# Kernel optimization log

Measured on AMD Instinct MI355X. Metric: run time of the kernel, lower is better.

## Reference

```python
import jax, jax.numpy as jnp
import numpy as np

NUM_ITEMS = 50000
NUM_USERS = 16384   # static number of user segments (total_user universe)
H0 = 512            # encoder_hidden_size[0]
LAT = 256           # bottleneck (encoder_hidden_size[-1] / decoder_hidden_size[0])
N = 262144          # observed interactions
NT = 262144         # target interactions


def setup_inputs() -> dict:
    key = jax.random.key(0)
    ks = jax.random.split(key, 14)

    def glorot(k, shape):
        fan_in, fan_out = shape[1], shape[0]
        lim = np.sqrt(6.0 / (fan_in + fan_out)).astype(np.float32)
        return jax.random.uniform(k, shape, jnp.float32, -lim, lim)

    return {
        "user": jax.random.randint(ks[0], (N,), 0, NUM_USERS, jnp.int32),
        "item": jax.random.randint(ks[1], (N,), 0, NUM_ITEMS, jnp.int32),
        "rating": jax.random.normal(ks[2], (N,), jnp.float32),
        "target_user": jax.random.randint(ks[3], (NT,), 0, NUM_USERS, jnp.int32),
        "target_item": jax.random.randint(ks[4], (NT,), 0, NUM_ITEMS, jnp.int32),
        "target_rating": jax.random.normal(ks[5], (NT,), jnp.float32),
        # encoder_linear: Linear(num_items, H0)
        "W_enc": glorot(ks[6], (H0, NUM_ITEMS)),
        "b_enc": jnp.zeros((H0,), jnp.float32),
        # Encoder: Linear(H0, LAT) + Tanh
        "W1": glorot(ks[7], (LAT, H0)),
        "b1": jnp.zeros((LAT,), jnp.float32),
        # Decoder: Linear(LAT, H0) + Tanh
        "W2": glorot(ks[8], (H0, LAT)),
        "b2": jnp.zeros((H0,), jnp.float32),
        # decoder_linear: Linear(H0, num_items)
        "W_dec": glorot(ks[9], (NUM_ITEMS, H0)),
        "b_dec": jnp.zeros((NUM_ITEMS,), jnp.float32),
    }


def reference(user, item, rating, target_user, target_item, target_rating,
              W_enc, b_enc, W1, b1, W2, b2, W_dec, b_dec):
    # --- encoder: gather item weight rows, scale by rating, segment-sum per user ---
    # rows: [N, H0] gather from W_enc.T ([NUM_ITEMS, H0])
    rows = W_enc.T[item] * rating[:, None]
    # per-user aggregation over the full user universe (equivalent to the
    # torch unique/sort/index_add path: users with no interactions get 0 -> tanh(bias))
    agg = jax.ops.segment_sum(rows, user, num_segments=NUM_USERS)  # [U, H0]
    x = jnp.tanh(agg + b_enc)
    # --- small dense tanh MLP encoder/decoder ---
    encoded = jnp.tanh(x @ W1.T + b1)          # [U, LAT]
    decoded = jnp.tanh(encoded @ W2.T + b2)    # [U, H0] (dropout = identity, eval mode)
    # --- decoder: gather user codes & item decoder rows, rowwise dot ---
    g = decoded[target_user]                   # [NT, H0]
    w = W_dec[target_item]                     # [NT, H0]
    pred = jnp.sum(g * w, axis=-1) + b_dec[target_item]  # [NT]
    loss = jnp.mean((pred - target_rating) ** 2)
    return pred, loss
```

## Files before the change

### kernel.cpp

```cpp
#include <hip/hip_runtime.h>
#include <hip/hip_bf16.h>
#include <math.h>

#define NUM_ITEMS 50000
#define NUM_USERS 16384
#define ITEM_BINS 65536
#define H0 512
#define LAT 256

typedef __attribute__((ext_vector_type(8))) short short8;
typedef __attribute__((ext_vector_type(4))) float floatx4;

__device__ __forceinline__ unsigned short f2bf(float f) {
    union { float f; unsigned i; } u; u.f = f;
    unsigned r = u.i + 0x7fff + ((u.i >> 16) & 1);
    return (unsigned short)(r >> 16);
}
__device__ __forceinline__ float bfhi(unsigned v) {
    union { unsigned i; float f; } u; u.i = v & 0xffff0000u; return u.f;
}
__device__ __forceinline__ float bflo(unsigned v) {
    union { unsigned i; float f; } u; u.i = v << 16; return u.f;
}
__device__ __forceinline__ uint4 pack8(const float* v) {
    uint4 p;
    p.x = (unsigned)f2bf(v[0]) | ((unsigned)f2bf(v[1]) << 16);
    p.y = (unsigned)f2bf(v[2]) | ((unsigned)f2bf(v[3]) << 16);
    p.z = (unsigned)f2bf(v[4]) | ((unsigned)f2bf(v[5]) << 16);
    p.w = (unsigned)f2bf(v[6]) | ((unsigned)f2bf(v[7]) << 16);
    return p;
}

__global__ __launch_bounds__(256) void setup_kernel(
        const float* __restrict__ W_enc, unsigned short* __restrict__ wtb,
        const float* __restrict__ W_dec, unsigned short* __restrict__ wdb,
        const float* __restrict__ W1, unsigned short* __restrict__ w1b,
        const float* __restrict__ W2, unsigned short* __restrict__ w2b,
        const int* __restrict__ user, int* __restrict__ cntU,
        const int* __restrict__ t_item, int* __restrict__ cntI,
        int n, int nt, int TB, int DB, int CB) {
    __shared__ float tile[64][65];
    int bid = blockIdx.x;
    int tid = threadIdx.x;
    if (bid < TB) {
        const int TBX = (NUM_ITEMS + 63) / 64;
        int bx = bid % TBX, by = bid / TBX;
        int x0 = bx * 64, y0 = by * 64;
        int tx = tid & 63, ty = tid >> 6;
        int x = x0 + tx;
        if (x < NUM_ITEMS) {
#pragma unroll
            for (int j = 0; j < 64; j += 4)
                tile[j + ty][tx] = W_enc[(size_t)(y0 + j + ty) * NUM_ITEMS + x];
        }
        __syncthreads();
#pragma unroll
        for (int j = 0; j < 64; j += 4) {
            int it = x0 + j + ty;
            if (it < NUM_ITEMS)
                wtb[(size_t)it * H0 + y0 + tx] = f2bf(tile[tx][j + ty]);
        }
    } else if (bid < TB + DB) {
        int idx = (bid - TB) * 2048 + tid * 8;
        float v[8];
        *(float4*)&v[0] = *(const float4*)(W_dec + idx);
        *(float4*)&v[4] = *(const float4*)(W_dec + idx + 4);
        *(uint4*)(wdb + idx) = pack8(v);
    } else if (bid < TB + DB + CB) {
        int i = (bid - TB - DB) * 1024 + tid * 4;
        if (i + 3 < n) {
            int4 u = *(const int4*)(user + i);
            atomicAdd(&cntU[u.x], 1); atomicAdd(&cntU[u.y], 1);
            atomicAdd(&cntU[u.z], 1); atomicAdd(&cntU[u.w], 1);
        } else {
            for (int k = i; k < n; ++k) atomicAdd(&cntU[user[k]], 1);
        }
        if (i + 3 < nt) {
            int4 t = *(const int4*)(t_item + i);
            atomicAdd(&cntI[t.x], 1); atomicAdd(&cntI[t.y], 1);
            atomicAdd(&cntI[t.z], 1); atomicAdd(&cntI[t.w], 1);
        } else {
            for (int k = i; k < nt; ++k) atomicAdd(&cntI[t_item[k]], 1);
        }
    } else {
        int b2i = bid - TB - DB - CB;
        const float* src = (b2i < 64) ? W1 : W2;
        unsigned short* dst = (b2i < 64) ? w1b : w2b;
        int idx = (b2i & 63) * 2048 + tid * 8;
        float v[8];
        *(float4*)&v[0] = *(const float4*)(src + idx);
        *(float4*)&v[4] = *(const float4*)(src + idx + 4);
        *(uint4*)(dst + idx) = pack8(v);
    }
}

__device__ void scan_block(const int* __restrict__ cnt, int* __restrict__ offs,
                           int* __restrict__ cursor, int per) {
    __shared__ int ssum[1024];
    int t = threadIdx.x;
    int base = t * per;
    int s = 0;
    for (int j = 0; j < per; j += 4) {
        int4 v = *(const int4*)(cnt + base + j);
        s += v.x + v.y + v.z + v.w;
    }
    ssum[t] = s;
    __syncthreads();
    for (int off = 1; off < 1024; off <<= 1) {
        int v = (t >= off) ? ssum[t - off] : 0;
        __syncthreads();
        ssum[t] += v;
        __syncthreads();
    }
    int run = (t == 0) ? 0 : ssum[t - 1];
    for (int j = 0; j < per; j += 4) {
        int4 v = *(const int4*)(cnt + base + j);
        int4 o;
        o.x = run; run += v.x;
        o.y = run; run += v.y;
        o.z = run; run += v.z;
        o.w = run; run += v.w;
        *(int4*)(offs + base + j) = o;
        *(int4*)(cursor + base + j) = o;
    }
}

__global__ void scan_kernel(const int* __restrict__ cntU, int* __restrict__ offsU, int* __restrict__ curU,
                            const int* __restrict__ cntI, int* __restrict__ offsI, int* __restrict__ curI) {
    if (blockIdx.x == 0) scan_block(cntU, offsU, curU, NUM_USERS / 1024);
    else scan_block(cntI, offsI, curI, ITEM_BINS / 1024);
}

__global__ void scatter_kernel(const int* __restrict__ user, const int* __restrict__ item,
                               const float* __restrict__ rating, int* __restrict__ curU,
                               int2* __restrict__ s_pack,
                               const int* __restrict__ t_user, const int* __restrict__ t_item,
                               const float* __restrict__ t_rating, int* __restrict__ curI,
                               int4* __restrict__ st_pack, int n, int nt) {
    int i = blockIdx.x * blockDim.x + threadIdx.x;
    if (i < n) {
        int u = user[i];
        int pos = atomicAdd(&curU[u], 1);
        s_pack[pos] = make_int2(item[i], __float_as_int(rating[i]));
    }
    if (i < nt) {
        int it = t_item[i];
        int pos = atomicAdd(&curI[it], 1);
        st_pack[pos] = make_int4(t_user[i], it, __float_as_int(t_rating[i]), i);
    }
}

__global__ __launch_bounds__(256) void agg_kernel(const unsigned short* __restrict__ wtb,
                                                  const int* __restrict__ offs,
                                                  const int* __restrict__ ends,
                                                  const int2* __restrict__ s_pack,
                                                  const float* __restrict__ b_enc,
                                                  unsigned short* __restrict__ xb) {
    __shared__ float red[3 * 512];
    int u = blockIdx.x;
    int tid = threadIdx.x;
    int g = tid >> 6, lane = tid & 63;
    float acc[8] = {};
    int j0 = offs[u], j1 = ends[u];
    int j = j0 + g;
    int2 nxt = (j < j1) ? s_pack[j] : make_int2(0, 0);
    while (j < j1) {
        int2 cur = nxt;
        int jn = j + 4;
        if (jn < j1) nxt = s_pack[jn];
        float r = __int_as_float(cur.y);
        uint4 v = ((const uint4*)(wtb + (size_t)cur.x * H0))[lane];
        acc[0] += bflo(v.x) * r; acc[1] += bfhi(v.x) * r;
        acc[2] += bflo(v.y) * r; acc[3] += bfhi(v.y) * r;
        acc[4] += bflo(v.z) * r; acc[5] += bfhi(v.z) * r;
        acc[6] += bflo(v.w) * r; acc[7] += bfhi(v.w) * r;
        j = jn;
    }
    if (g) {
        float4* rp = (float4*)red + (size_t)(g - 1) * 128 + lane * 2;
        rp[0] = make_float4(acc[0], acc[1], acc[2], acc[3]);
        rp[1] = make_float4(acc[4], acc[5], acc[6], acc[7]);
    }
    __syncthreads();
    if (g == 0) {
#pragma unroll
        for (int h = 0; h < 3; ++h) {
            const float* rp = red + h * 512 + lane * 8;
#pragma unroll
            for (int e = 0; e < 8; ++e) acc[e] += rp[e];
        }
        float4 b0 = ((const float4*)b_enc)[lane * 2];
        float4 b1 = ((const float4*)b_enc)[lane * 2 + 1];
        float o[8];
        o[0] = tanhf(acc[0] + b0.x); o[1] = tanhf(acc[1] + b0.y);
        o[2] = tanhf(acc[2] + b0.z); o[3] = tanhf(acc[3] + b0.w);
        o[4] = tanhf(acc[4] + b1.x); o[5] = tanhf(acc[5] + b1.y);
        o[6] = tanhf(acc[6] + b1.z); o[7] = tanhf(acc[7] + b1.w);
        ((uint4*)(xb + (size_t)u * H0))[lane] = pack8(o);
    }
}

template<int BN>
__global__ __launch_bounds__(256) void gemm_mfma(const unsigned short* __restrict__ A,
                                                 const unsigned short* __restrict__ B,
                                                 const float* __restrict__ bias,
                                                 unsigned short* __restrict__ C,
                                                 int Nn, int K) {
    constexpr int WN = BN / 32;
    constexpr int NCH = 8 + BN / 16;
    constexpr int PER = NCH / 4;
    __shared__ unsigned short Ash[128 * 32];
    __shared__ unsigned short Bsh[BN * 32];
    int tid = threadIdx.x;
    int wid = tid >> 6, lane = tid & 63;
    int wave_m = wid & 1, wave_n = wid >> 1;
    int quad = lane >> 4, l16 = lane & 15;
    int m0 = blockIdx.x * 128, n0 = blockIdx.y * BN;
    floatx4 acc[4][WN] = {};
    int srow = lane >> 2;
    int scol = (lane & 3) * 8;
    for (int k0 = 0; k0 < K; k0 += 32) {
#pragma unroll
        for (int i = 0; i < PER; ++i) {
            int c = wid * PER + i;
            if (c < 8) {
                const unsigned short* ga = A + (size_t)(m0 + c * 16 + srow) * K + k0 + scol;
                __builtin_amdgcn_global_load_lds(
                    (const __attribute__((address_space(1))) void*)ga,
                    (__attribute__((address_space(3))) void*)((__attribute__((address_space(3))) char*)Ash + c * 1024),
                    16, 0, 0);
            } else {
                const unsigned short* gb = B + (size_t)(n0 + (c - 8) * 16 + srow) * K + k0 + scol;
                __builtin_amdgcn_global_load_lds(
                    (const __attribute__((address_space(1))) void*)gb,
                    (__attribute__((address_space(3))) void*)((__attribute__((address_space(3))) char*)Bsh + (c - 8) * 1024),
                    16, 0, 0);
            }
        }
        __syncthreads();
        short8 af[4], bfr[WN];
#pragma unroll
        for (int i = 0; i < 4; ++i) {
            int ml = wave_m * 64 + i * 16 + l16;
            af[i] = ((const short8*)Ash)[ml * 4 + quad];
        }
#pragma unroll
        for (int j = 0; j < WN; ++j) {
            int nl = wave_n * (BN / 2) + j * 16 + l16;
            bfr[j] = ((const short8*)Bsh)[nl * 4 + quad];
        }
#pragma unroll
        for (int i = 0; i < 4; ++i)
#pragma unroll
            for (int j = 0; j < WN; ++j)
                acc[i][j] = __builtin_amdgcn_mfma_f32_16x16x32_bf16(af[i], bfr[j], acc[i][j], 0, 0, 0);
        __syncthreads();
    }
#pragma unroll
    for (int j = 0; j < WN; ++j) {
        int col = n0 + wave_n * (BN / 2) + j * 16 + l16;
        float bv = bias[col];
#pragma unroll
        for (int i = 0; i < 4; ++i) {
            int rowb = m0 + wave_m * 64 + i * 16 + quad * 4;
#pragma unroll
            for (int r = 0; r < 4; ++r)
                C[(size_t)(rowb + r) * Nn + col] = f2bf(tanhf(acc[i][j][r] + bv));
        }
    }
}

__global__ __launch_bounds__(256) void predict_kernel(const unsigned short* __restrict__ dec_b,
                                                      const unsigned short* __restrict__ wdb,
                                                      const float* __restrict__ b_dec,
                                                      const int4* __restrict__ st,
                                                      float* __restrict__ pred,
                                                      float* __restrict__ partials, int NT) {
    __shared__ float wsum[4];
    int wid = threadIdx.x >> 6, lane = threadIdx.x & 63;
    int base = (blockIdx.x * 4 + wid) * 4;
    float sq = 0.f;
    int4 tv[4];
    uint4 gv[4], wv[4];
#pragma unroll
    for (int t = 0; t < 4; ++t) tv[t] = st[min(base + t, NT - 1)];
#pragma unroll
    for (int t = 0; t < 4; ++t) {
        gv[t] = ((const uint4*)(dec_b + (size_t)tv[t].x * H0))[lane];
        wv[t] = ((const uint4*)(wdb + (size_t)tv[t].y * H0))[lane];
    }
#pragma unroll
    for (int t = 0; t < 4; ++t) {
        float s = bflo(gv[t].x) * bflo(wv[t].x) + bfhi(gv[t].x) * bfhi(wv[t].x)
                + bflo(gv[t].y) * bflo(wv[t].y) + bfhi(gv[t].y) * bfhi(wv[t].y)
                + bflo(gv[t].z) * bflo(wv[t].z) + bfhi(gv[t].z) * bfhi(wv[t].z)
                + bflo(gv[t].w) * bflo(wv[t].w) + bfhi(gv[t].w) * bfhi(wv[t].w);
#pragma unroll
        for (int off = 32; off; off >>= 1) s += __shfl_xor(s, off, 64);
        if (lane == 0 && base + t < NT) {
            float p = s + b_dec[tv[t].y];
            pred[tv[t].w] = p;
            float d = p - __int_as_float(tv[t].z);
            sq += d * d;
        }
    }
    if (lane == 0) wsum[wid] = sq;
    __syncthreads();
    if (threadIdx.x == 0) partials[blockIdx.x] = wsum[0] + wsum[1] + wsum[2] + wsum[3];
}

__global__ void loss_reduce(const float* __restrict__ partials, float* __restrict__ out_loss,
                            int nPart, float invNT) {
    __shared__ float s[256];
    int t = threadIdx.x;
    float a = 0.f;
    const float4* p4 = (const float4*)partials;
    int n4 = nPart >> 2;
    for (int i = t; i < n4; i += 256) {
        float4 v = p4[i];
        a += v.x + v.y + v.z + v.w;
    }
    for (int i = (n4 << 2) + t; i < nPart; i += 256) a += partials[i];
    s[t] = a;
    __syncthreads();
    for (int off = 128; off; off >>= 1) {
        if (t < off) s[t] += s[t + off];
        __syncthreads();
    }
    if (t == 0) out_loss[0] = s[0] * invNT;
}

extern "C" void kernel_launch(void* const* d_in, const int* in_sizes, int n_in,
                              void* d_out, int out_size, void* d_ws, size_t ws_size,
                              hipStream_t stream) {
    const int* user = (const int*)d_in[0];
    const int* item = (const int*)d_in[1];
    const float* rating = (const float*)d_in[2];
    const int* t_user = (const int*)d_in[3];
    const int* t_item = (const int*)d_in[4];
    const float* t_rating = (const float*)d_in[5];
    const float* W_enc = (const float*)d_in[6];
    const float* b_enc = (const float*)d_in[7];
    const float* W1 = (const float*)d_in[8];
    const float* b1 = (const float*)d_in[9];
    const float* W2 = (const float*)d_in[10];
    const float* b2 = (const float*)d_in[11];
    const float* W_dec = (const float*)d_in[12];
    const float* b_dec = (const float*)d_in[13];
    const int N = in_sizes[0];
    const int NT = in_sizes[3];

    char* ws = (char*)d_ws;
    size_t off = 0;
    auto alloc = [&](size_t bytes) {
        void* p = ws + off;
        off = (off + bytes + 255) & ~(size_t)255;
        return p;
    };
    unsigned short* wtb = (unsigned short*)alloc((size_t)NUM_ITEMS * H0 * 2);
    unsigned short* wdb = (unsigned short*)alloc((size_t)NUM_ITEMS * H0 * 2);
    unsigned short* xb = (unsigned short*)alloc((size_t)NUM_USERS * H0 * 2);
    unsigned short* enc_b = (unsigned short*)alloc((size_t)NUM_USERS * LAT * 2);
    unsigned short* dec_b = (unsigned short*)alloc((size_t)NUM_USERS * H0 * 2);
    unsigned short* w1b = (unsigned short*)alloc((size_t)LAT * H0 * 2);
    unsigned short* w2b = (unsigned short*)alloc((size_t)H0 * LAT * 2);
    int* cntU = (int*)alloc((size_t)(NUM_USERS + ITEM_BINS) * 4);
    int* cntI = cntU + NUM_USERS;
    int* offsU = (int*)alloc((size_t)NUM_USERS * 4);
    int* curU = (int*)alloc((size_t)NUM_USERS * 4);
    int* offsI = (int*)alloc((size_t)ITEM_BINS * 4);
    int* curI = (int*)alloc((size_t)ITEM_BINS * 4);
    int2* s_pack = (int2*)alloc((size_t)N * 8);
    int4* st_pack = (int4*)alloc((size_t)NT * 16);
    const int predBlocks = (NT + 15) / 16;
    float* partials = (float*)alloc((size_t)predBlocks * 4);

    float* pred = (float*)d_out;
    float* loss = pred + NT;

    const int maxNNT = N > NT ? N : NT;
    const int TBX = (NUM_ITEMS + 63) / 64;
    const int TB = TBX * (H0 / 64);
    const int DB = (NUM_ITEMS * H0) / 2048;
    const int CB = (maxNNT + 1023) / 1024;
    const int WB = 128;

    hipMemsetAsync(cntU, 0, (size_t)(NUM_USERS + ITEM_BINS) * 4, stream);
    setup_kernel<<<TB + DB + CB + WB, 256, 0, stream>>>(
        W_enc, wtb, W_dec, wdb, W1, w1b, W2, w2b,
        user, cntU, t_item, cntI, N, NT, TB, DB, CB);
    scan_kernel<<<2, 1024, 0, stream>>>(cntU, offsU, curU, cntI, offsI, curI);
    scatter_kernel<<<(maxNNT + 255) / 256, 256, 0, stream>>>(
        user, item, rating, curU, s_pack,
        t_user, t_item, t_rating, curI, st_pack, N, NT);
    agg_kernel<<<NUM_USERS, 256, 0, stream>>>(wtb, offsU, curU, s_pack, b_enc, xb);
    gemm_mfma<64><<<dim3(NUM_USERS / 128, LAT / 64), 256, 0, stream>>>(xb, w1b, b1, enc_b, LAT, H0);
    gemm_mfma<64><<<dim3(NUM_USERS / 128, H0 / 64), 256, 0, stream>>>(enc_b, w2b, b2, dec_b, H0, LAT);
    predict_kernel<<<predBlocks, 256, 0, stream>>>(dec_b, wdb, b_dec, st_pack, pred, partials, NT);
    loss_reduce<<<1, 256, 0, stream>>>(partials, loss, predBlocks, 1.0f / NT);
}
```

Baseline: 463.4 us.

## Store encoder/decoder weight tables as scaled FP8 and fuse setup with scatter

W_enc (transposed) and W_dec are now converted to FP8 with a fixed scale of 64 instead of bf16. This halves the bytes gathered per row in the aggregation and prediction kernels and halves the conversion writes. The conversion work moves into one kernel that also does the scatter, so the weight conversion overlaps with the scatter. The counting pass gets its own small kernel, and the transpose now uses float4 loads into a 64x128 tile. FP8 with a fixed scale loses accuracy and may fall outside the tolerance.

```diff
diff --git a/kernel.cpp b/kernel.cpp
--- a/kernel.cpp
+++ b/kernel.cpp
@@ -7,9 +7,12 @@
 #define ITEM_BINS 65536
 #define H0 512
 #define LAT 256
+#define FP8_SCALE 64.0f
+#define FP8_INV (1.0f / 64.0f)
 
 typedef __attribute__((ext_vector_type(8))) short short8;
 typedef __attribute__((ext_vector_type(4))) float floatx4;
+typedef __attribute__((ext_vector_type(2))) float vf2;
 
 __device__ __forceinline__ unsigned short f2bf(float f) {
     union { float f; unsigned i; } u; u.f = f;
@@ -30,67 +33,34 @@
     p.w = (unsigned)f2bf(v[6]) | ((unsigned)f2bf(v[7]) << 16);
     return p;
 }
-
-__global__ __launch_bounds__(256) void setup_kernel(
-        const float* __restrict__ W_enc, unsigned short* __restrict__ wtb,
-        const float* __restrict__ W_dec, unsigned short* __restrict__ wdb,
-        const float* __restrict__ W1, unsigned short* __restrict__ w1b,
-        const float* __restrict__ W2, unsigned short* __restrict__ w2b,
-        const int* __restrict__ user, int* __restrict__ cntU,
-        const int* __restrict__ t_item, int* __restrict__ cntI,
-        int n, int nt, int TB, int DB, int CB) {
-    __shared__ float tile[64][65];
-    int bid = blockIdx.x;
-    int tid = threadIdx.x;
-    if (bid < TB) {
-        const int TBX = (NUM_ITEMS + 63) / 64;
-        int bx = bid % TBX, by = bid / TBX;
-        int x0 = bx * 64, y0 = by * 64;
-        int tx = tid & 63, ty = tid >> 6;
-        int x = x0 + tx;
-        if (x < NUM_ITEMS) {
-#pragma unroll
-            for (int j = 0; j < 64; j += 4)
-                tile[j + ty][tx] = W_enc[(size_t)(y0 + j + ty) * NUM_ITEMS + x];
-        }
-        __syncthreads();
-#pragma unroll
-        for (int j = 0; j < 64; j += 4) {
-            int it = x0 + j + ty;
-            if (it < NUM_ITEMS)
-                wtb[(size_t)it * H0 + y0 + tx] = f2bf(tile[tx][j + ty]);
-        }
-    } else if (bid < TB + DB) {
-        int idx = (bid - TB) * 2048 + tid * 8;
-        float v[8];
-        *(float4*)&v[0] = *(const float4*)(W_dec + idx);
-        *(float4*)&v[4] = *(const float4*)(W_dec + idx + 4);
-        *(uint4*)(wdb + idx) = pack8(v);
-    } else if (bid < TB + DB + CB) {
-        int i = (bid - TB - DB) * 1024 + tid * 4;
-        if (i + 3 < n) {
-            int4 u = *(const int4*)(user + i);
-            atomicAdd(&cntU[u.x], 1); atomicAdd(&cntU[u.y], 1);
-            atomicAdd(&cntU[u.z], 1); atomicAdd(&cntU[u.w], 1);
-        } else {
-            for (int k = i; k < n; ++k) atomicAdd(&cntU[user[k]], 1);
-        }
-        if (i + 3 < nt) {
-            int4 t = *(const int4*)(t_item + i);
-            atomicAdd(&cntI[t.x], 1); atomicAdd(&cntI[t.y], 1);
-            atomicAdd(&cntI[t.z], 1); atomicAdd(&cntI[t.w], 1);
-        } else {
-            for (int k = i; k < nt; ++k) atomicAdd(&cntI[t_item[k]], 1);
-        }
+__device__ __forceinline__ unsigned pkfp8_4(float a, float b, float c, float d) {
+    int v = __builtin_amdgcn_cvt_pk_fp8_f32(a, b, 0, false);
+    v = __builtin_amdgcn_cvt_pk_fp8_f32(c, d, v, true);
+    return (unsigned)v;
+}
+__device__ __forceinline__ void fp8x4_to_f32(unsigned v, float* o) {
+    vf2 lo = __builtin_amdgcn_cvt_pk_f32_fp8((int)v, false);
+    vf2 hi = __builtin_amdgcn_cvt_pk_f32_fp8((int)v, true);
+    o[0] = lo.x; o[1] = lo.y; o[2] = hi.x; o[3] = hi.y;
+}
+
+__global__ __launch_bounds__(256) void count_kernel(const int* __restrict__ user, int* __restrict__ cntU,
+                                                    const int* __restrict__ t_item, int* __restrict__ cntI,
+                                                    int n, int nt) {
+    int i = (blockIdx.x * blockDim.x + threadIdx.x) * 4;
+    if (i + 3 < n) {
+        int4 u = *(const int4*)(user + i);
+        atomicAdd(&cntU[u.x], 1); atomicAdd(&cntU[u.y], 1);
+        atomicAdd(&cntU[u.z], 1); atomicAdd(&cntU[u.w], 1);
     } else {
-        int b2i = bid - TB - DB - CB;
-        const float* src = (b2i < 64) ? W1 : W2;
-        unsigned short* dst = (b2i < 64) ? w1b : w2b;
-        int idx = (b2i & 63) * 2048 + tid * 8;
-        float v[8];
-        *(float4*)&v[0] = *(const float4*)(src + idx);
-        *(float4*)&v[4] = *(const float4*)(src + idx + 4);
-        *(uint4*)(dst + idx) = pack8(v);
+        for (int k = i; k < n; ++k) atomicAdd(&cntU[user[k]], 1);
+    }
+    if (i + 3 < nt) {
+        int4 t = *(const int4*)(t_item + i);
+        atomicAdd(&cntI[t.x], 1); atomicAdd(&cntI[t.y], 1);
+        atomicAdd(&cntI[t.z], 1); atomicAdd(&cntI[t.w], 1);
+    } else {
+        for (int k = i; k < nt; ++k) atomicAdd(&cntI[t_item[k]], 1);
     }
 }
 
@@ -131,26 +101,93 @@
     else scan_block(cntI, offsI, curI, ITEM_BINS / 1024);
 }
 
-__global__ void scatter_kernel(const int* __restrict__ user, const int* __restrict__ item,
-                               const float* __restrict__ rating, int* __restrict__ curU,
-                               int2* __restrict__ s_pack,
-                               const int* __restrict__ t_user, const int* __restrict__ t_item,
-                               const float* __restrict__ t_rating, int* __restrict__ curI,
-                               int4* __restrict__ st_pack, int n, int nt) {
-    int i = blockIdx.x * blockDim.x + threadIdx.x;
-    if (i < n) {
-        int u = user[i];
-        int pos = atomicAdd(&curU[u], 1);
-        s_pack[pos] = make_int2(item[i], __float_as_int(rating[i]));
-    }
-    if (i < nt) {
-        int it = t_item[i];
-        int pos = atomicAdd(&curI[it], 1);
-        st_pack[pos] = make_int4(t_user[i], it, __float_as_int(t_rating[i]), i);
-    }
-}
-
-__global__ __launch_bounds__(256) void agg_kernel(const unsigned short* __restrict__ wtb,
+__global__ __launch_bounds__(256) void mega_kernel(
+        const int* __restrict__ user, const int* __restrict__ item,
+        const float* __restrict__ rating, int* __restrict__ curU, int2* __restrict__ s_pack,
+        const int* __restrict__ t_user, const int* __restrict__ t_item,
+        const float* __restrict__ t_rating, int* __restrict__ curI, int4* __restrict__ st_pack,
+        const float* __restrict__ W_enc, unsigned char* __restrict__ wtb8,
+        const float* __restrict__ W_dec, unsigned char* __restrict__ wdb8,
+        const float* __restrict__ W1, unsigned short* __restrict__ w1b,
+        const float* __restrict__ W2, unsigned short* __restrict__ w2b,
+        int n, int nt, int SB, int TB, int DB) {
+    __shared__ float tileT[64 * 129];
+    int bid = blockIdx.x;
+    int tid = threadIdx.x;
+    if (bid < SB) {
+        int i = bid * 256 + tid;
+        if (i < n) {
+            int u = user[i];
+            int pos = atomicAdd(&curU[u], 1);
+            s_pack[pos] = make_int2(item[i], __float_as_int(rating[i]));
+        }
+        if (i < nt) {
+            int it = t_item[i];
+            int pos = atomicAdd(&curI[it], 1);
+            st_pack[pos] = make_int4(t_user[i], it, __float_as_int(t_rating[i]), i);
+        }
+    } else if (bid < SB + TB) {
+        const int TBX = (NUM_ITEMS + 63) / 64;
+        int b = bid - SB;
+        int x0 = (b % TBX) * 64;
+        int y0 = (b / TBX) * 128;
+        int g = tid >> 4;
+        int m = tid & 15;
+        int ibase = m * 4;
+#pragma unroll
+        for (int p = 0; p < 8; ++p) {
+            int hloc = p * 16 + g;
+            int it = x0 + ibase;
+            if (it < NUM_ITEMS) {
+                float4 v = *(const float4*)(W_enc + (size_t)(y0 + hloc) * NUM_ITEMS + it);
+                tileT[(ibase + 0) * 129 + hloc] = v.x;
+                tileT[(ibase + 1) * 129 + hloc] = v.y;
+                tileT[(ibase + 2) * 129 + hloc] = v.z;
+                tileT[(ibase + 3) * 129 + hloc] = v.w;
+            }
+        }
+        __syncthreads();
+        int l = tid & 7;
+        int i0 = tid >> 3;
+#pragma unroll
+        for (int p = 0; p < 2; ++p) {
+            int i = p * 32 + i0;
+            int it = x0 + i;
+            if (it < NUM_ITEMS) {
+                const float* src = tileT + i * 129 + l * 16;
+                uint4 o;
+                o.x = pkfp8_4(src[0] * FP8_SCALE, src[1] * FP8_SCALE, src[2] * FP8_SCALE, src[3] * FP8_SCALE);
+                o.y = pkfp8_4(src[4] * FP8_SCALE, src[5] * FP8_SCALE, src[6] * FP8_SCALE, src[7] * FP8_SCALE);
+                o.z = pkfp8_4(src[8] * FP8_SCALE, src[9] * FP8_SCALE, src[10] * FP8_SCALE, src[11] * FP8_SCALE);
+                o.w = pkfp8_4(src[12] * FP8_SCALE, src[13] * FP8_SCALE, src[14] * FP8_SCALE, src[15] * FP8_SCALE);
+                *(uint4*)(wtb8 + (size_t)it * H0 + y0 + l * 16) = o;
+            }
+        }
+    } else if (bid < SB + TB + DB) {
+        size_t idx = (size_t)(bid - SB - TB) * 4096 + tid * 16;
+        float4 v0 = *(const float4*)(W_dec + idx);
+        float4 v1 = *(const float4*)(W_dec + idx + 4);
+        float4 v2 = *(const float4*)(W_dec + idx + 8);
+        float4 v3 = *(const float4*)(W_dec + idx + 12);
+        uint4 o;
+        o.x = pkfp8_4(v0.x * FP8_SCALE, v0.y * FP8_SCALE, v0.z * FP8_SCALE, v0.w * FP8_SCALE);
+        o.y = pkfp8_4(v1.x * FP8_SCALE, v1.y * FP8_SCALE, v1.z * FP8_SCALE, v1.w * FP8_SCALE);
+        o.z = pkfp8_4(v2.x * FP8_SCALE, v2.y * FP8_SCALE, v2.z * FP8_SCALE, v2.w * FP8_SCALE);
+        o.w = pkfp8_4(v3.x * FP8_SCALE, v3.y * FP8_SCALE, v3.z * FP8_SCALE, v3.w * FP8_SCALE);
+        *(uint4*)(wdb8 + idx) = o;
+    } else {
+        int b2i = bid - SB - TB - DB;
+        const float* src = (b2i < 64) ? W1 : W2;
+        unsigned short* dst = (b2i < 64) ? w1b : w2b;
+        int idx = (b2i & 63) * 2048 + tid * 8;
+        float v[8];
+        *(float4*)&v[0] = *(const float4*)(src + idx);
+        *(float4*)&v[4] = *(const float4*)(src + idx + 4);
+        *(uint4*)(dst + idx) = pack8(v);
+    }
+}
+
+__global__ __launch_bounds__(256) void agg_kernel(const unsigned char* __restrict__ wtb8,
                                                   const int* __restrict__ offs,
                                                   const int* __restrict__ ends,
                                                   const int2* __restrict__ s_pack,
@@ -169,11 +206,12 @@
         int jn = j + 4;
         if (jn < j1) nxt = s_pack[jn];
         float r = __int_as_float(cur.y);
-        uint4 v = ((const uint4*)(wtb + (size_t)cur.x * H0))[lane];
-        acc[0] += bflo(v.x) * r; acc[1] += bfhi(v.x) * r;
-        acc[2] += bflo(v.y) * r; acc[3] += bfhi(v.y) * r;
-        acc[4] += bflo(v.z) * r; acc[5] += bfhi(v.z) * r;
-        acc[6] += bflo(v.w) * r; acc[7] += bfhi(v.w) * r;
+        uint2 v = ((const uint2*)(wtb8 + (size_t)cur.x * H0))[lane];
+        float wf[8];
+        fp8x4_to_f32(v.x, wf);
+        fp8x4_to_f32(v.y, wf + 4);
+#pragma unroll
+        for (int e = 0; e < 8; ++e) acc[e] += wf[e] * r;
         j = jn;
     }
     if (g) {
@@ -192,10 +230,10 @@
         float4 b0 = ((const float4*)b_enc)[lane * 2];
         float4 b1 = ((const float4*)b_enc)[lane * 2 + 1];
         float o[8];
-        o[0] = tanhf(acc[0] + b0.x); o[1] = tanhf(acc[1] + b0.y);
-        o[2] = tanhf(acc[2] + b0.z); o[3] = tanhf(acc[3] + b0.w);
-        o[4] = tanhf(acc[4] + b1.x); o[5] = tanhf(acc[5] + b1.y);
-        o[6] = tanhf(acc[6] + b1.z); o[7] = tanhf(acc[7] + b1.w);
+        o[0] = tanhf(acc[0] * FP8_INV + b0.x); o[1] = tanhf(acc[1] * FP8_INV + b0.y);
+        o[2] = tanhf(acc[2] * FP8_INV + b0.z); o[3] = tanhf(acc[3] * FP8_INV + b0.w);
+        o[4] = tanhf(acc[4] * FP8_INV + b1.x); o[5] = tanhf(acc[5] * FP8_INV + b1.y);
+        o[6] = tanhf(acc[6] * FP8_INV + b1.z); o[7] = tanhf(acc[7] * FP8_INV + b1.w);
         ((uint4*)(xb + (size_t)u * H0))[lane] = pack8(o);
     }
 }
@@ -271,7 +309,7 @@
 }
 
 __global__ __launch_bounds__(256) void predict_kernel(const unsigned short* __restrict__ dec_b,
-                                                      const unsigned short* __restrict__ wdb,
+                                                      const unsigned char* __restrict__ wdb8,
                                                       const float* __restrict__ b_dec,
                                                       const int4* __restrict__ st,
                                                       float* __restrict__ pred,
@@ -281,24 +319,28 @@
     int base = (blockIdx.x * 4 + wid) * 4;
     float sq = 0.f;
     int4 tv[4];
-    uint4 gv[4], wv[4];
+    uint4 gv[4];
+    uint2 wv[4];
 #pragma unroll
     for (int t = 0; t < 4; ++t) tv[t] = st[min(base + t, NT - 1)];
 #pragma unroll
     for (int t = 0; t < 4; ++t) {
         gv[t] = ((const uint4*)(dec_b + (size_t)tv[t].x * H0))[lane];
-        wv[t] = ((const uint4*)(wdb + (size_t)tv[t].y * H0))[lane];
+        wv[t] = ((const uint2*)(wdb8 + (size_t)tv[t].y * H0))[lane];
     }
 #pragma unroll
     for (int t = 0; t < 4; ++t) {
-        float s = bflo(gv[t].x) * bflo(wv[t].x) + bfhi(gv[t].x) * bfhi(wv[t].x)
-                + bflo(gv[t].y) * bflo(wv[t].y) + bfhi(gv[t].y) * bfhi(wv[t].y)
-                + bflo(gv[t].z) * bflo(wv[t].z) + bfhi(gv[t].z) * bfhi(wv[t].z)
-                + bflo(gv[t].w) * bflo(wv[t].w) + bfhi(gv[t].w) * bfhi(wv[t].w);
+        float wf[8];
+        fp8x4_to_f32(wv[t].x, wf);
+        fp8x4_to_f32(wv[t].y, wf + 4);
+        float s = bflo(gv[t].x) * wf[0] + bfhi(gv[t].x) * wf[1]
+                + bflo(gv[t].y) * wf[2] + bfhi(gv[t].y) * wf[3]
+                + bflo(gv[t].z) * wf[4] + bfhi(gv[t].z) * wf[5]
+                + bflo(gv[t].w) * wf[6] + bfhi(gv[t].w) * wf[7];
 #pragma unroll
         for (int off = 32; off; off >>= 1) s += __shfl_xor(s, off, 64);
         if (lane == 0 && base + t < NT) {
-            float p = s + b_dec[tv[t].y];
+            float p = s * FP8_INV + b_dec[tv[t].y];
             pred[tv[t].w] = p;
             float d = p - __int_as_float(tv[t].z);
             sq += d * d;
@@ -357,8 +399,8 @@
         off = (off + bytes + 255) & ~(size_t)255;
         return p;
     };
-    unsigned short* wtb = (unsigned short*)alloc((size_t)NUM_ITEMS * H0 * 2);
-    unsigned short* wdb = (unsigned short*)alloc((size_t)NUM_ITEMS * H0 * 2);
+    unsigned char* wtb8 = (unsigned char*)alloc((size_t)NUM_ITEMS * H0);
+    unsigned char* wdb8 = (unsigned char*)alloc((size_t)NUM_ITEMS * H0);
     unsigned short* xb = (unsigned short*)alloc((size_t)NUM_USERS * H0 * 2);
     unsigned short* enc_b = (unsigned short*)alloc((size_t)NUM_USERS * LAT * 2);
     unsigned short* dec_b = (unsigned short*)alloc((size_t)NUM_USERS * H0 * 2);
@@ -379,23 +421,23 @@
     float* loss = pred + NT;
 
     const int maxNNT = N > NT ? N : NT;
+    const int SB = (maxNNT + 255) / 256;
     const int TBX = (NUM_ITEMS + 63) / 64;
-    const int TB = TBX * (H0 / 64);
-    const int DB = (NUM_ITEMS * H0) / 2048;
-    const int CB = (maxNNT + 1023) / 1024;
+    const int TB = TBX * (H0 / 128);
+    const int DB = (NUM_ITEMS * H0) / 4096;
     const int WB = 128;
 
     hipMemsetAsync(cntU, 0, (size_t)(NUM_USERS + ITEM_BINS) * 4, stream);
-    setup_kernel<<<TB + DB + CB + WB, 256, 0, stream>>>(
-        W_enc, wtb, W_dec, wdb, W1, w1b, W2, w2b,
-        user, cntU, t_item, cntI, N, NT, TB, DB, CB);
+    count_kernel<<<(maxNNT + 1023) / 1024, 256, 0, stream>>>(user, cntU, t_item, cntI, N, NT);
     scan_kernel<<<2, 1024, 0, stream>>>(cntU, offsU, curU, cntI, offsI, curI);
-    scatter_kernel<<<(maxNNT + 255) / 256, 256, 0, stream>>>(
+    mega_kernel<<<SB + TB + DB + WB, 256, 0, stream>>>(
         user, item, rating, curU, s_pack,
-        t_user, t_item, t_rating, curI, st_pack, N, NT);
-    agg_kernel<<<NUM_USERS, 256, 0, stream>>>(wtb, offsU, curU, s_pack, b_enc, xb);
+        t_user, t_item, t_rating, curI, st_pack,
+        W_enc, wtb8, W_dec, wdb8, W1, w1b, W2, w2b,
+        N, NT, SB, TB, DB);
+    agg_kernel<<<NUM_USERS, 256, 0, stream>>>(wtb8, offsU, curU, s_pack, b_enc, xb);
     gemm_mfma<64><<<dim3(NUM_USERS / 128, LAT / 64), 256, 0, stream>>>(xb, w1b, b1, enc_b, LAT, H0);
     gemm_mfma<64><<<dim3(NUM_USERS / 128, H0 / 64), 256, 0, stream>>>(enc_b, w2b, b2, dec_b, H0, LAT);
-    predict_kernel<<<predBlocks, 256, 0, stream>>>(dec_b, wdb, b_dec, st_pack, pred, partials, NT);
+    predict_kernel<<<predBlocks, 256, 0, stream>>>(dec_b, wdb8, b_dec, st_pack, pred, partials, NT);
     loss_reduce<<<1, 256, 0, stream>>>(partials, loss, predBlocks, 1.0f / NT);
 }
```

Result: faster. 450.9 us (-2.7%).
